# Kernel optimization log

Hardware: AMD Instinct MI355X
Metric: run time of the kernel (lower is better)

Reference implementation:

```python
import jax, jax.numpy as jnp
import numpy as np

B, N, M, C = 4, 4096, 4096, 256
IMG_W, IMG_H = 1242.0, 376.0  # KITTI-like image extents for keypoint coords


def setup_inputs() -> dict:
    key = jax.random.key(0)
    ks = jax.random.split(key, 12)
    s = 1.0 / np.sqrt(C)
    scale_uv = jnp.array([IMG_W, IMG_H], dtype=jnp.float32)
    return {
        "nodes_L": jax.random.normal(ks[0], (B, N, C), jnp.float32),
        "nodes_R": jax.random.normal(ks[1], (B, M, C), jnp.float32),
        "kpts_L": jax.random.uniform(ks[2], (B, N, 2), jnp.float32) * scale_uv,
        "kpts_R": jax.random.uniform(ks[3], (B, M, 2), jnp.float32) * scale_uv,
        "Wq": jax.random.normal(ks[4], (C, C), jnp.float32) * s,
        "bq": jnp.zeros((C,), jnp.float32),
        "Wk": jax.random.normal(ks[5], (C, C), jnp.float32) * s,
        "bk": jnp.zeros((C,), jnp.float32),
        "Wv": jax.random.normal(ks[6], (C, C), jnp.float32) * s,
        "bv": jnp.zeros((C,), jnp.float32),
        "Wm": jax.random.normal(ks[7], (C, C), jnp.float32) * s,
        "bm": jnp.zeros((C,), jnp.float32),
    }


def reference(nodes_L, nodes_R, kpts_L, kpts_R, Wq, bq, Wk, bk, Wv, bv, Wm, bm):
    dim = nodes_L.shape[-1]
    # torch.nn.Linear: y = x @ W.T + b  (W is [out, in])
    Q = jnp.einsum('bnc,dc->bnd', nodes_L, Wq) + bq  # [B,N,C]
    K = jnp.einsum('bmc,dc->bmd', nodes_R, Wk) + bk  # [B,M,C]
    V = jnp.einsum('bmc,dc->bmd', nodes_R, Wv) + bv  # [B,M,C]

    # Epipolar geometric mask from keypoint coordinates
    dist_v = jnp.abs(kpts_L[:, :, 1:2] - kpts_R[:, None, :, 1])  # [B,N,M]
    dist_u = kpts_L[:, :, 0:1] - kpts_R[:, None, :, 0]           # [B,N,M]
    mask = (dist_v < 3.0) & (dist_u > 0) & (dist_u < 192)

    attn = jnp.einsum('bnd,bmd->bnm', Q, K) / (dim ** 0.5)       # [B,N,M]
    attn = jnp.where(mask, attn, jnp.float32(-1e9))
    attn_weights = jax.nn.softmax(attn, axis=-1)                 # [B,N,M]

    matched_features = jnp.einsum('bnm,bmd->bnd', attn_weights, V)
    init_disparity = jnp.sum(attn_weights * dist_u, axis=-1, keepdims=True)  # [B,N,1]
    confidence = jnp.any(mask, axis=-1, keepdims=True).astype(jnp.float32)   # [B,N,1]
    out = jnp.einsum('bnd,cd->bnc', matched_features, Wm) + bm   # [B,N,C]
    return (out, init_disparity, confidence, attn_weights)
```

## Files before the change

### kernel.cpp

```cpp
#include <hip/hip_runtime.h>
#include <stdint.h>

#define CAP 192

typedef __attribute__((ext_vector_type(4))) float f32x4;
typedef __attribute__((ext_vector_type(8))) short bf16x8;

__device__ __forceinline__ float bf2f(ushort u) {
  return __uint_as_float(((unsigned)u) << 16);
}
__device__ __forceinline__ ushort f2bf(float f) {
  unsigned u = __float_as_uint(f);
  return (ushort)((u + 0x7fffu + ((u >> 16) & 1u)) >> 16);
}
__device__ __forceinline__ float wredsum(float v) {
#pragma unroll
  for (int o = 32; o; o >>= 1) v += __shfl_xor(v, o);
  return v;
}

__global__ __launch_bounds__(256) void cvt_kernel(const float* __restrict__ s,
                                                  ushort* __restrict__ d, int n4) {
  int i = blockIdx.x * 256 + threadIdx.x;
  if (i < n4) {
    float4 v = *(const float4*)(s + (size_t)i * 4);
    ushort4 o = { f2bf(v.x), f2bf(v.y), f2bf(v.z), f2bf(v.w) };
    *(ushort4*)(d + (size_t)i * 4) = o;
  }
}

__global__ __launch_bounds__(256) void cvt4_kernel(
    const float* __restrict__ s0, const float* __restrict__ s1,
    const float* __restrict__ s2, const float* __restrict__ s3,
    ushort* __restrict__ d0, ushort* __restrict__ d1,
    ushort* __restrict__ d2, ushort* __restrict__ d3) {
  int seg = blockIdx.x >> 6;
  int i = ((blockIdx.x & 63) * 256 + threadIdx.x) * 4;
  const float* s = (seg == 0) ? s0 : (seg == 1) ? s1 : (seg == 2) ? s2 : s3;
  ushort* d = (seg == 0) ? d0 : (seg == 1) ? d1 : (seg == 2) ? d2 : d3;
  float4 v = *(const float4*)(s + i);
  ushort4 o = { f2bf(v.x), f2bf(v.y), f2bf(v.z), f2bf(v.w) };
  *(ushort4*)(d + i) = o;
}

template <typename OutT>
__device__ __forceinline__ void gemm_body(const ushort* __restrict__ A,
                                          const ushort* __restrict__ W,
                                          const float* __restrict__ bias,
                                          OutT* __restrict__ Y, int blk,
                                          ushort* As, ushort* Bs) {
  int tid = threadIdx.x;
  int lane = tid & 63, wid = tid >> 6;
  int bm = blk >> 1, bn = blk & 1;
  int r0 = bm * 128, c0 = bn * 128;
  int wr = wid >> 1, wc = wid & 1;
  f32x4 acc[4][4] = {};
  for (int k0 = 0; k0 < 256; k0 += 32) {
    __syncthreads();
#pragma unroll
    for (int p = 0; p < 2; ++p) {
      int u = p * 2048 + tid * 8;
      int row = u >> 5, col = u & 31;
      *(bf16x8*)&As[u] = *(const bf16x8*)(A + (size_t)(r0 + row) * 256 + k0 + col);
      *(bf16x8*)&Bs[u] = *(const bf16x8*)(W + (size_t)(c0 + row) * 256 + k0 + col);
    }
    __syncthreads();
    bf16x8 af[4], bfr[4];
    int rsel = lane & 15, ksel = (lane >> 4) * 8;
#pragma unroll
    for (int m = 0; m < 4; ++m)
      af[m] = *(bf16x8*)&As[(wr * 64 + m * 16 + rsel) * 32 + ksel];
#pragma unroll
    for (int n = 0; n < 4; ++n)
      bfr[n] = *(bf16x8*)&Bs[(wc * 64 + n * 16 + rsel) * 32 + ksel];
#pragma unroll
    for (int m = 0; m < 4; ++m)
#pragma unroll
      for (int n = 0; n < 4; ++n)
        acc[m][n] = __builtin_amdgcn_mfma_f32_16x16x32_bf16(af[m], bfr[n], acc[m][n], 0, 0, 0);
  }
  int rbase = r0 + wr * 64 + ((lane >> 4) * 4);
  int cbase = c0 + wc * 64 + (lane & 15);
#pragma unroll
  for (int n = 0; n < 4; ++n) {
    float bv = bias[cbase + n * 16];
#pragma unroll
    for (int m = 0; m < 4; ++m) {
#pragma unroll
      for (int j = 0; j < 4; ++j) {
        float v = acc[m][n][j] + bv;
        size_t idx = (size_t)(rbase + m * 16 + j) * 256 + (cbase + n * 16);
        if constexpr (sizeof(OutT) == 2) Y[idx] = (OutT)f2bf(v);
        else Y[idx] = (OutT)v;
      }
    }
  }
}

__global__ __launch_bounds__(256, 2) void gemm3(
    const ushort* __restrict__ Xl, const ushort* __restrict__ Xr,
    const ushort* __restrict__ Wqb, const ushort* __restrict__ Wkb,
    const ushort* __restrict__ Wvb, const float* __restrict__ bq,
    const float* __restrict__ bk, const float* __restrict__ bv,
    ushort* __restrict__ Qb, ushort* __restrict__ Kb, ushort* __restrict__ Vb) {
  __shared__ __align__(16) ushort As[128 * 32];
  __shared__ __align__(16) ushort Bs[128 * 32];
  int which = blockIdx.x >> 8;
  int blk = blockIdx.x & 255;
  const ushort* A = (which == 0) ? Xl : Xr;
  const ushort* W = (which == 0) ? Wqb : (which == 1) ? Wkb : Wvb;
  const float* bias = (which == 0) ? bq : (which == 1) ? bk : bv;
  ushort* Y = (which == 0) ? Qb : (which == 1) ? Kb : Vb;
  gemm_body<ushort>(A, W, bias, Y, blk, As, Bs);
}

__global__ __launch_bounds__(256, 2) void gemm_out(const ushort* __restrict__ A,
                                                   const ushort* __restrict__ W,
                                                   const float* __restrict__ bias,
                                                   float* __restrict__ Y) {
  __shared__ __align__(16) ushort As[128 * 32];
  __shared__ __align__(16) ushort Bs[128 * 32];
  gemm_body<float>(A, W, bias, Y, blockIdx.x, As, Bs);
}

__global__ __launch_bounds__(256) void sum_nodes(const float* __restrict__ nodesR,
                                                 const float* __restrict__ kptsR,
                                                 float* __restrict__ S,
                                                 float* __restrict__ sumU) {
  int b = blockIdx.x >> 4, ch = blockIdx.x & 15;
  int t = threadIdx.x;
  int c4 = (t & 63) * 4;
  int r0 = b * 4096 + ch * 256 + (t >> 6);
  float4 acc = {0.f, 0.f, 0.f, 0.f};
  for (int k = 0; k < 64; ++k) {
    float4 v = *(const float4*)(nodesR + (size_t)(r0 + k * 4) * 256 + c4);
    acc.x += v.x; acc.y += v.y; acc.z += v.z; acc.w += v.w;
  }
  __shared__ float4 red[256];
  red[t] = acc;
  float u = kptsR[(size_t)(b * 4096 + ch * 256 + t) * 2];
  u = wredsum(u);
  __shared__ float ured[4];
  if ((t & 63) == 0) ured[t >> 6] = u;
  __syncthreads();
  if (t < 64) {
    float4 x = red[t], y = red[t + 64], z = red[t + 128], w = red[t + 192];
    atomicAdd(&S[b * 256 + c4 + 0], x.x + y.x + z.x + w.x);
    atomicAdd(&S[b * 256 + c4 + 1], x.y + y.y + z.y + w.y);
    atomicAdd(&S[b * 256 + c4 + 2], x.z + y.z + z.z + w.z);
    atomicAdd(&S[b * 256 + c4 + 3], x.w + y.w + z.w + w.w);
  }
  if (t == 0) atomicAdd(&sumU[b], ured[0] + ured[1] + ured[2] + ured[3]);
}

__global__ __launch_bounds__(256) void proj_mean(const float* __restrict__ S,
                                                 const float* __restrict__ sumU,
                                                 const float* __restrict__ Wv,
                                                 const float* __restrict__ bv,
                                                 ushort* __restrict__ meanVb,
                                                 float* __restrict__ meanU) {
  int b = blockIdx.x, c = threadIdx.x;
  const float* s = S + b * 256;
  float acc = 0.f;
  for (int k = 0; k < 256; k += 4) {
    float4 w = *(const float4*)(Wv + (size_t)c * 256 + k);
    acc += s[k] * w.x + s[k + 1] * w.y + s[k + 2] * w.z + s[k + 3] * w.w;
  }
  float mv = acc * (1.f / 4096.f) + bv[c];
  meanVb[b * 256 + c] = f2bf(mv);
  if (c == 0) meanU[b] = sumU[b] * (1.f / 4096.f);
}

__global__ __launch_bounds__(512, 2) void attn_rows(
    const float* __restrict__ kptsL, const float* __restrict__ kptsR,
    const ushort* __restrict__ Qb, const ushort* __restrict__ Kb,
    const ushort* __restrict__ Vb, const float* __restrict__ meanU,
    const ushort* __restrict__ meanVb, float* __restrict__ disp_out,
    float* __restrict__ conf_out, ushort* __restrict__ matched,
    int* __restrict__ rowcnt, int2* __restrict__ rowlist) {
  __shared__ float2 kR[4096];
  __shared__ int bufM[8][CAP];
  __shared__ float bufD[8][CAP];
  __shared__ float bufS[8][CAP];
  int tid = threadIdx.x, lane = tid & 63, wid = tid >> 6;
  int b = blockIdx.x >> 9;
  int n = ((blockIdx.x & 511) << 3) + wid;
  int row = (b << 12) + n;
  int bb = b << 12;
  const float2* kRsrc = (const float2*)kptsR + (size_t)bb;
  for (int i = tid; i < 4096; i += 512) kR[i] = kRsrc[i];
  __syncthreads();
  float2 kL = ((const float2*)kptsL)[(size_t)row];
  ushort4 qv = *(const ushort4*)(Qb + (size_t)row * 256 + lane * 4);
  float q0 = bf2f(qv.x), q1 = bf2f(qv.y), q2 = bf2f(qv.z), q3 = bf2f(qv.w);

  int cnt = 0;
  for (int m0 = 0; m0 < 4096; m0 += 64) {
    float2 kr = kR[m0 + lane];
    float dv = fabsf(kL.y - kr.y);
    float du = kL.x - kr.x;
    bool hit = (dv < 3.0f) && (du > 0.0f) && (du < 192.0f);
    unsigned long long bal = __ballot(hit);
    if (bal) {
      if (hit) {
        int pos = cnt + (int)__popcll(bal & ((1ull << lane) - 1ull));
        if (pos < CAP) { bufM[wid][pos] = m0 + lane; bufD[wid][pos] = du; }
      }
      cnt += (int)__popcll(bal);
    }
  }
  if (cnt > CAP) cnt = CAP;

  float conf, disp;
  if (cnt == 0) {
    conf = 0.f;
    disp = kL.x - meanU[b];
    if (lane == 0) rowcnt[row] = 0;
    ushort4 st = *(const ushort4*)(meanVb + b * 256 + lane * 4);
    *(ushort4*)(matched + (size_t)row * 256 + lane * 4) = st;
  } else {
    float mx = -1e30f;
    int i = 0;
    for (; i + 1 < cnt; i += 2) {
      int ma = bufM[wid][i], mb = bufM[wid][i + 1];
      ushort4 ka = *(const ushort4*)(Kb + ((size_t)(bb + ma)) * 256 + lane * 4);
      ushort4 kb2 = *(const ushort4*)(Kb + ((size_t)(bb + mb)) * 256 + lane * 4);
      float pa = q0 * bf2f(ka.x) + q1 * bf2f(ka.y) + q2 * bf2f(ka.z) + q3 * bf2f(ka.w);
      float pb = q0 * bf2f(kb2.x) + q1 * bf2f(kb2.y) + q2 * bf2f(kb2.z) + q3 * bf2f(kb2.w);
#pragma unroll
      for (int o = 32; o; o >>= 1) {
        pa += __shfl_xor(pa, o);
        pb += __shfl_xor(pb, o);
      }
      float sa = pa * 0.0625f, sb = pb * 0.0625f;
      if (lane == 0) { bufS[wid][i] = sa; bufS[wid][i + 1] = sb; }
      mx = fmaxf(mx, fmaxf(sa, sb));
    }
    if (i < cnt) {
      int ma = bufM[wid][i];
      ushort4 ka = *(const ushort4*)(Kb + ((size_t)(bb + ma)) * 256 + lane * 4);
      float pa = q0 * bf2f(ka.x) + q1 * bf2f(ka.y) + q2 * bf2f(ka.z) + q3 * bf2f(ka.w);
      pa = wredsum(pa);
      float sa = pa * 0.0625f;
      if (lane == 0) bufS[wid][i] = sa;
      mx = fmaxf(mx, sa);
    }
    float psum = 0.f, pdisp = 0.f;
    for (int k = lane; k < cnt; k += 64) {
      float e = expf(bufS[wid][k] - mx);
      bufS[wid][k] = e;
      psum += e;
      pdisp += e * bufD[wid][k];
    }
    psum = wredsum(psum);
    pdisp = wredsum(pdisp);
    float inv = 1.f / psum;
    disp = pdisp * inv;
    conf = 1.f;
    for (int k = lane; k < cnt; k += 64) {
      int2 e;
      e.x = bufM[wid][k];
      e.y = __float_as_int(bufS[wid][k] * inv);
      rowlist[(size_t)row * CAP + k] = e;
    }
    if (lane == 0) rowcnt[row] = cnt;
    float a0 = 0.f, a1 = 0.f, a2 = 0.f, a3 = 0.f;
    i = 0;
    for (; i + 1 < cnt; i += 2) {
      float wa = bufS[wid][i] * inv, wb = bufS[wid][i + 1] * inv;
      int ma = bufM[wid][i], mb = bufM[wid][i + 1];
      ushort4 va = *(const ushort4*)(Vb + ((size_t)(bb + ma)) * 256 + lane * 4);
      ushort4 vb2 = *(const ushort4*)(Vb + ((size_t)(bb + mb)) * 256 + lane * 4);
      a0 += wa * bf2f(va.x) + wb * bf2f(vb2.x);
      a1 += wa * bf2f(va.y) + wb * bf2f(vb2.y);
      a2 += wa * bf2f(va.z) + wb * bf2f(vb2.z);
      a3 += wa * bf2f(va.w) + wb * bf2f(vb2.w);
    }
    if (i < cnt) {
      float wa = bufS[wid][i] * inv;
      int ma = bufM[wid][i];
      ushort4 va = *(const ushort4*)(Vb + ((size_t)(bb + ma)) * 256 + lane * 4);
      a0 += wa * bf2f(va.x); a1 += wa * bf2f(va.y);
      a2 += wa * bf2f(va.z); a3 += wa * bf2f(va.w);
    }
    ushort4 st = { f2bf(a0), f2bf(a1), f2bf(a2), f2bf(a3) };
    *(ushort4*)(matched + (size_t)row * 256 + lane * 4) = st;
  }
  if (lane == 0) { disp_out[row] = disp; conf_out[row] = conf; }
}

__global__ __launch_bounds__(256) void fill_attn(const int* __restrict__ rowcnt,
                                                 float* __restrict__ attn) {
  int r0 = blockIdx.x * 8;
  int tid = threadIdx.x;
#pragma unroll
  for (int r = 0; r < 8; ++r) {
    int row = r0 + r;
    float fill = (rowcnt[row] == 0) ? (1.f / 4096.f) : 0.f;
    f32x4 fv = { fill, fill, fill, fill };
    f32x4* dst = (f32x4*)(attn + (size_t)row * 4096);
#pragma unroll
    for (int j = 0; j < 4; ++j)
      __builtin_nontemporal_store(fv, dst + j * 256 + tid);
  }
}

__global__ __launch_bounds__(256) void scatter_attn(const int* __restrict__ rowcnt,
                                                    const int2* __restrict__ rowlist,
                                                    float* __restrict__ attn) {
  int row = blockIdx.x * 4 + (threadIdx.x >> 6);
  int lane = threadIdx.x & 63;
  int cnt = rowcnt[row];
  for (int i = lane; i < cnt; i += 64) {
    int2 e = rowlist[(size_t)row * CAP + i];
    attn[(size_t)row * 4096 + e.x] = __int_as_float(e.y);
  }
}

extern "C" void kernel_launch(void* const* d_in, const int* in_sizes, int n_in,
                              void* d_out, int out_size, void* d_ws, size_t ws_size,
                              hipStream_t stream) {
  const float* nodes_L = (const float*)d_in[0];
  const float* nodes_R = (const float*)d_in[1];
  const float* kpts_L = (const float*)d_in[2];
  const float* kpts_R = (const float*)d_in[3];
  const float* Wq = (const float*)d_in[4];
  const float* bq = (const float*)d_in[5];
  const float* Wk = (const float*)d_in[6];
  const float* bk = (const float*)d_in[7];
  const float* Wv = (const float*)d_in[8];
  const float* bv = (const float*)d_in[9];
  const float* Wm = (const float*)d_in[10];
  const float* bm = (const float*)d_in[11];

  float* out = (float*)d_out;
  float* disp = out + 4194304;
  float* conf = disp + 16384;
  float* attn = conf + 16384;

  char* ws = (char*)d_ws;
  ushort* Xl = (ushort*)(ws + 0);
  ushort* Xr = (ushort*)(ws + 8388608);
  ushort* Wqb = (ushort*)(ws + 16777216);
  ushort* Wkb = Wqb + 65536;
  ushort* Wvb = Wkb + 65536;
  ushort* Wmb = Wvb + 65536;
  ushort* Qb = (ushort*)(ws + 17301504);
  ushort* Kb = (ushort*)(ws + 25690112);
  ushort* Vb = (ushort*)(ws + 34078720);
  ushort* matched = (ushort*)(ws + 42467328);
  float* S = (float*)(ws + 50855936);
  float* sumU = (float*)(ws + 50860032);
  float* meanU = (float*)(ws + 50860096);
  ushort* meanVb = (ushort*)(ws + 50860160);
  int* rowcnt = (int*)(ws + 50864128);
  int2* rowlist = (int2*)(ws + 50929664);

  (void)hipMemsetAsync(S, 0, 4096 + 64, stream);
  cvt_kernel<<<4096, 256, 0, stream>>>(nodes_L, Xl, 1048576);
  cvt_kernel<<<4096, 256, 0, stream>>>(nodes_R, Xr, 1048576);
  cvt4_kernel<<<256, 256, 0, stream>>>(Wq, Wk, Wv, Wm, Wqb, Wkb, Wvb, Wmb);
  sum_nodes<<<64, 256, 0, stream>>>(nodes_R, kpts_R, S, sumU);
  gemm3<<<768, 256, 0, stream>>>(Xl, Xr, Wqb, Wkb, Wvb, bq, bk, bv, Qb, Kb, Vb);
  proj_mean<<<4, 256, 0, stream>>>(S, sumU, Wv, bv, meanVb, meanU);
  attn_rows<<<2048, 512, 0, stream>>>(kpts_L, kpts_R, Qb, Kb, Vb, meanU, meanVb,
                                      disp, conf, matched, rowcnt, rowlist);
  fill_attn<<<2048, 256, 0, stream>>>(rowcnt, attn);
  scatter_attn<<<4096, 256, 0, stream>>>(rowcnt, rowlist, attn);
  gemm_out<<<256, 256, 0, stream>>>(matched, Wmb, bm, out);
}
```

Baseline: 460.2 us.

## Fuse fp32-to-bf16 conversion into GEMM tile loads and drop separate cvt kernels

Removes the three standalone conversion kernels and instead converts fp32 node and weight tiles to bf16 while staging them into shared memory inside the GEMMs. This avoids writing and rereading bf16 copies of the inputs and saves three launches, but each GEMM tile load now reads fp32, twice the bytes, and weights get re-converted per block. The epipolar scan loop is also made branch-free and unrolled, and scatter_attn uses a grid-stride loop over fewer blocks.

```diff
diff --git a/kernel.cpp b/kernel.cpp
--- a/kernel.cpp
+++ b/kernel.cpp
@@ -19,33 +19,9 @@
   return v;
 }
 
-__global__ __launch_bounds__(256) void cvt_kernel(const float* __restrict__ s,
-                                                  ushort* __restrict__ d, int n4) {
-  int i = blockIdx.x * 256 + threadIdx.x;
-  if (i < n4) {
-    float4 v = *(const float4*)(s + (size_t)i * 4);
-    ushort4 o = { f2bf(v.x), f2bf(v.y), f2bf(v.z), f2bf(v.w) };
-    *(ushort4*)(d + (size_t)i * 4) = o;
-  }
-}
-
-__global__ __launch_bounds__(256) void cvt4_kernel(
-    const float* __restrict__ s0, const float* __restrict__ s1,
-    const float* __restrict__ s2, const float* __restrict__ s3,
-    ushort* __restrict__ d0, ushort* __restrict__ d1,
-    ushort* __restrict__ d2, ushort* __restrict__ d3) {
-  int seg = blockIdx.x >> 6;
-  int i = ((blockIdx.x & 63) * 256 + threadIdx.x) * 4;
-  const float* s = (seg == 0) ? s0 : (seg == 1) ? s1 : (seg == 2) ? s2 : s3;
-  ushort* d = (seg == 0) ? d0 : (seg == 1) ? d1 : (seg == 2) ? d2 : d3;
-  float4 v = *(const float4*)(s + i);
-  ushort4 o = { f2bf(v.x), f2bf(v.y), f2bf(v.z), f2bf(v.w) };
-  *(ushort4*)(d + i) = o;
-}
-
-template <typename OutT>
-__device__ __forceinline__ void gemm_body(const ushort* __restrict__ A,
-                                          const ushort* __restrict__ W,
+template <bool A_BF16, typename OutT>
+__device__ __forceinline__ void gemm_body(const void* __restrict__ Av,
+                                          const float* __restrict__ Wf,
                                           const float* __restrict__ bias,
                                           OutT* __restrict__ Y, int blk,
                                           ushort* As, ushort* Bs) {
@@ -61,8 +37,26 @@
     for (int p = 0; p < 2; ++p) {
       int u = p * 2048 + tid * 8;
       int row = u >> 5, col = u & 31;
-      *(bf16x8*)&As[u] = *(const bf16x8*)(A + (size_t)(r0 + row) * 256 + k0 + col);
-      *(bf16x8*)&Bs[u] = *(const bf16x8*)(W + (size_t)(c0 + row) * 256 + k0 + col);
+      if constexpr (A_BF16) {
+        *(bf16x8*)&As[u] =
+            *(const bf16x8*)((const ushort*)Av + (size_t)(r0 + row) * 256 + k0 + col);
+      } else {
+        const float* Af = (const float*)Av;
+        float4 lo = *(const float4*)(Af + (size_t)(r0 + row) * 256 + k0 + col);
+        float4 hi = *(const float4*)(Af + (size_t)(r0 + row) * 256 + k0 + col + 4);
+        ushort4 o0 = { f2bf(lo.x), f2bf(lo.y), f2bf(lo.z), f2bf(lo.w) };
+        ushort4 o1 = { f2bf(hi.x), f2bf(hi.y), f2bf(hi.z), f2bf(hi.w) };
+        *(ushort4*)&As[u] = o0;
+        *(ushort4*)&As[u + 4] = o1;
+      }
+      {
+        float4 lo = *(const float4*)(Wf + (size_t)(c0 + row) * 256 + k0 + col);
+        float4 hi = *(const float4*)(Wf + (size_t)(c0 + row) * 256 + k0 + col + 4);
+        ushort4 o0 = { f2bf(lo.x), f2bf(lo.y), f2bf(lo.z), f2bf(lo.w) };
+        ushort4 o1 = { f2bf(hi.x), f2bf(hi.y), f2bf(hi.z), f2bf(hi.w) };
+        *(ushort4*)&Bs[u] = o0;
+        *(ushort4*)&Bs[u + 4] = o1;
+      }
     }
     __syncthreads();
     bf16x8 af[4], bfr[4];
@@ -98,29 +92,29 @@
 }
 
 __global__ __launch_bounds__(256, 2) void gemm3(
-    const ushort* __restrict__ Xl, const ushort* __restrict__ Xr,
-    const ushort* __restrict__ Wqb, const ushort* __restrict__ Wkb,
-    const ushort* __restrict__ Wvb, const float* __restrict__ bq,
+    const float* __restrict__ nodesL, const float* __restrict__ nodesR,
+    const float* __restrict__ Wq, const float* __restrict__ Wk,
+    const float* __restrict__ Wv, const float* __restrict__ bq,
     const float* __restrict__ bk, const float* __restrict__ bv,
     ushort* __restrict__ Qb, ushort* __restrict__ Kb, ushort* __restrict__ Vb) {
   __shared__ __align__(16) ushort As[128 * 32];
   __shared__ __align__(16) ushort Bs[128 * 32];
   int which = blockIdx.x >> 8;
   int blk = blockIdx.x & 255;
-  const ushort* A = (which == 0) ? Xl : Xr;
-  const ushort* W = (which == 0) ? Wqb : (which == 1) ? Wkb : Wvb;
+  const float* A = (which == 0) ? nodesL : nodesR;
+  const float* W = (which == 0) ? Wq : (which == 1) ? Wk : Wv;
   const float* bias = (which == 0) ? bq : (which == 1) ? bk : bv;
   ushort* Y = (which == 0) ? Qb : (which == 1) ? Kb : Vb;
-  gemm_body<ushort>(A, W, bias, Y, blk, As, Bs);
+  gemm_body<false, ushort>(A, W, bias, Y, blk, As, Bs);
 }
 
 __global__ __launch_bounds__(256, 2) void gemm_out(const ushort* __restrict__ A,
-                                                   const ushort* __restrict__ W,
+                                                   const float* __restrict__ Wm,
                                                    const float* __restrict__ bias,
                                                    float* __restrict__ Y) {
   __shared__ __align__(16) ushort As[128 * 32];
   __shared__ __align__(16) ushort Bs[128 * 32];
-  gemm_body<float>(A, W, bias, Y, blockIdx.x, As, Bs);
+  gemm_body<true, float>(A, Wm, bias, Y, blockIdx.x, As, Bs);
 }
 
 __global__ __launch_bounds__(256) void sum_nodes(const float* __restrict__ nodesR,
@@ -194,20 +188,18 @@
   ushort4 qv = *(const ushort4*)(Qb + (size_t)row * 256 + lane * 4);
   float q0 = bf2f(qv.x), q1 = bf2f(qv.y), q2 = bf2f(qv.z), q3 = bf2f(qv.w);
 
+  unsigned long long lmask = (1ull << lane) - 1ull;
   int cnt = 0;
+#pragma unroll 4
   for (int m0 = 0; m0 < 4096; m0 += 64) {
     float2 kr = kR[m0 + lane];
     float dv = fabsf(kL.y - kr.y);
     float du = kL.x - kr.x;
     bool hit = (dv < 3.0f) && (du > 0.0f) && (du < 192.0f);
     unsigned long long bal = __ballot(hit);
-    if (bal) {
-      if (hit) {
-        int pos = cnt + (int)__popcll(bal & ((1ull << lane) - 1ull));
-        if (pos < CAP) { bufM[wid][pos] = m0 + lane; bufD[wid][pos] = du; }
-      }
-      cnt += (int)__popcll(bal);
-    }
+    int pos = cnt + (int)__popcll(bal & lmask);
+    if (hit && pos < CAP) { bufM[wid][pos] = m0 + lane; bufD[wid][pos] = du; }
+    cnt += (int)__popcll(bal);
   }
   if (cnt > CAP) cnt = CAP;
 
@@ -308,12 +300,13 @@
 __global__ __launch_bounds__(256) void scatter_attn(const int* __restrict__ rowcnt,
                                                     const int2* __restrict__ rowlist,
                                                     float* __restrict__ attn) {
-  int row = blockIdx.x * 4 + (threadIdx.x >> 6);
   int lane = threadIdx.x & 63;
-  int cnt = rowcnt[row];
-  for (int i = lane; i < cnt; i += 64) {
-    int2 e = rowlist[(size_t)row * CAP + i];
-    attn[(size_t)row * 4096 + e.x] = __int_as_float(e.y);
+  for (int row = blockIdx.x * 4 + (threadIdx.x >> 6); row < 16384; row += gridDim.x * 4) {
+    int cnt = rowcnt[row];
+    for (int i = lane; i < cnt; i += 64) {
+      int2 e = rowlist[(size_t)row * CAP + i];
+      attn[(size_t)row * 4096 + e.x] = __int_as_float(e.y);
+    }
   }
 }
 
@@ -339,33 +332,24 @@
   float* attn = conf + 16384;
 
   char* ws = (char*)d_ws;
-  ushort* Xl = (ushort*)(ws + 0);
-  ushort* Xr = (ushort*)(ws + 8388608);
-  ushort* Wqb = (ushort*)(ws + 16777216);
-  ushort* Wkb = Wqb + 65536;
-  ushort* Wvb = Wkb + 65536;
-  ushort* Wmb = Wvb + 65536;
-  ushort* Qb = (ushort*)(ws + 17301504);
-  ushort* Kb = (ushort*)(ws + 25690112);
-  ushort* Vb = (ushort*)(ws + 34078720);
-  ushort* matched = (ushort*)(ws + 42467328);
-  float* S = (float*)(ws + 50855936);
-  float* sumU = (float*)(ws + 50860032);
-  float* meanU = (float*)(ws + 50860096);
-  ushort* meanVb = (ushort*)(ws + 50860160);
-  int* rowcnt = (int*)(ws + 50864128);
-  int2* rowlist = (int2*)(ws + 50929664);
+  ushort* Qb = (ushort*)(ws + 0);
+  ushort* Kb = (ushort*)(ws + 8388608);
+  ushort* Vb = (ushort*)(ws + 16777216);
+  ushort* matched = (ushort*)(ws + 25165824);
+  float* S = (float*)(ws + 33554432);
+  float* sumU = (float*)(ws + 33558528);
+  float* meanU = (float*)(ws + 33558592);
+  ushort* meanVb = (ushort*)(ws + 33558656);
+  int* rowcnt = (int*)(ws + 33562624);
+  int2* rowlist = (int2*)(ws + 33628160);
 
   (void)hipMemsetAsync(S, 0, 4096 + 64, stream);
-  cvt_kernel<<<4096, 256, 0, stream>>>(nodes_L, Xl, 1048576);
-  cvt_kernel<<<4096, 256, 0, stream>>>(nodes_R, Xr, 1048576);
-  cvt4_kernel<<<256, 256, 0, stream>>>(Wq, Wk, Wv, Wm, Wqb, Wkb, Wvb, Wmb);
   sum_nodes<<<64, 256, 0, stream>>>(nodes_R, kpts_R, S, sumU);
-  gemm3<<<768, 256, 0, stream>>>(Xl, Xr, Wqb, Wkb, Wvb, bq, bk, bv, Qb, Kb, Vb);
+  gemm3<<<768, 256, 0, stream>>>(nodes_L, nodes_R, Wq, Wk, Wv, bq, bk, bv, Qb, Kb, Vb);
   proj_mean<<<4, 256, 0, stream>>>(S, sumU, Wv, bv, meanVb, meanU);
   attn_rows<<<2048, 512, 0, stream>>>(kpts_L, kpts_R, Qb, Kb, Vb, meanU, meanVb,
                                       disp, conf, matched, rowcnt, rowlist);
   fill_attn<<<2048, 256, 0, stream>>>(rowcnt, attn);
-  scatter_attn<<<4096, 256, 0, stream>>>(rowcnt, rowlist, attn);
-  gemm_out<<<256, 256, 0, stream>>>(matched, Wmb, bm, out);
-}
+  scatter_attn<<<512, 256, 0, stream>>>(rowcnt, rowlist, attn);
+  gemm_out<<<256, 256, 0, stream>>>(matched, Wm, bm, out);
+}
```

Result: slower. 481.8 us (+4.7%).
